# Kernel optimization log

Hardware: AMD Instinct MI355X
Metric: run time of the kernel (lower is better)

Reference implementation:

```python
import jax, jax.numpy as jnp
import numpy as np

N = 50000      # nodes
E = 800000     # edges (avg degree 16)
D = 64         # input/hidden dim
OUT = 1        # output head dim
ATT_SLOPE = 0.2   # PyG GATConv leaky_relu slope for attention logits
ACT_SLOPE = 0.01  # nn.LeakyReLU default slope


def _gat_layer(x, src, dst, W, a_src, a_dst, b, n):
    """PyG GATConv, heads=1, concat=True, with self-loops already in src/dst."""
    h = x @ W.T                                   # [n, D]
    logit = jax.nn.leaky_relu(h[src] @ a_src + h[dst] @ a_dst, ATT_SLOPE)  # [e]
    m = jax.ops.segment_max(logit, dst, num_segments=n)                    # per-dst max
    e = jnp.exp(logit - m[dst])
    denom = jax.ops.segment_sum(e, dst, num_segments=n)
    coef = e / denom[dst]                         # softmax over incoming edges
    out = jax.ops.segment_sum(coef[:, None] * h[src], dst, num_segments=n)
    return out + b


def setup_inputs() -> dict:
    key = jax.random.key(0)
    ks = jax.random.split(key, 16)
    s = 1.0 / np.sqrt(D)
    inp = {"x": jax.random.normal(ks[0], (N, D), dtype=jnp.float32)}
    for i in range(3):
        inp[f"W{i}"] = jax.random.normal(ks[1 + 4 * i], (D, D), dtype=jnp.float32) * s
        inp[f"a_src{i}"] = jax.random.normal(ks[2 + 4 * i], (D,), dtype=jnp.float32) * s
        inp[f"a_dst{i}"] = jax.random.normal(ks[3 + 4 * i], (D,), dtype=jnp.float32) * s
        inp[f"b{i}"] = jnp.zeros((D,), dtype=jnp.float32)
    inp["Wout"] = jax.random.normal(ks[13], (OUT, D), dtype=jnp.float32) * s
    inp["bout"] = jnp.zeros((OUT,), dtype=jnp.float32)
    inp["edge_index"] = jax.random.randint(ks[14], (2, E), 0, N, dtype=jnp.int64)
    return inp


def reference(x, W0, a_src0, a_dst0, b0, W1, a_src1, a_dst1, b1,
              W2, a_src2, a_dst2, b2, Wout, bout, edge_index):
    n = x.shape[0]
    loops = jnp.arange(n, dtype=edge_index.dtype)
    src = jnp.concatenate([edge_index[0], loops])  # GATConv add_self_loops=True
    dst = jnp.concatenate([edge_index[1], loops])
    act = lambda v: jax.nn.leaky_relu(v, ACT_SLOPE)
    h = act(_gat_layer(x, src, dst, W0, a_src0, a_dst0, b0, n))
    h = act(_gat_layer(h, src, dst, W1, a_src1, a_dst1, b1, n))
    h = act(_gat_layer(h, src, dst, W2, a_src2, a_dst2, b2, n))
    return h @ Wout.T + bout                       # [n, OUT]
```

## Files before the change

### kernel.cpp

```cpp
#include <hip/hip_runtime.h>
#include <hip/hip_fp16.h>

#define DD 64
#define ATT_SLOPE 0.2f
#define ACT_SLOPE 0.01f
#define GNPB 32
#define RCAP 64
#define PA_CHUNK 2048
#define BSH 8
#define BNODES 256
#define BCAP 5888

template <bool IN_HALF>
__device__ __forceinline__ void gemm_body(
        const void* __restrict__ in_, const float* __restrict__ W,
        const float* __restrict__ a_src, const float* __restrict__ a_dst,
        __half* __restrict__ h, float* __restrict__ as_out,
        float* __restrict__ ad_out, int n_nodes, int base, float* xin) {
    int t = threadIdx.x;
    int lane = t & 63;
    int w = t >> 6;
    if (IN_HALF) {
        const uint2* src = (const uint2*)in_;
        float4* xin4 = (float4*)xin;
        int lim = n_nodes * (DD / 4);
        #pragma unroll
        for (int i = 0; i < 2; ++i) {
            int idx = i * 256 + t;
            int gi = base * (DD / 4) + idx;
            uint2 v = {0, 0};
            if (gi < lim) v = src[gi];
            float2 f0 = __half22float2(*(const __half2*)&v.x);
            float2 f1 = __half22float2(*(const __half2*)&v.y);
            xin4[idx] = make_float4(f0.x, f0.y, f1.x, f1.y);
        }
    } else {
        float4* xin4 = (float4*)xin;
        const float4* src4 = (const float4*)in_;
        int lim = n_nodes * (DD / 4);
        #pragma unroll
        for (int i = 0; i < (GNPB * DD / 4) / 256; ++i) {
            int idx = i * 256 + t;
            int gi = base * (DD / 4) + idx;
            xin4[idx] = (gi < lim) ? src4[gi]
                                   : make_float4(0.f, 0.f, 0.f, 0.f);
        }
    }
    __syncthreads();

    int n0 = base + w * 8;
    if (n0 >= n_nodes) return;

    float asl = a_src[lane], adl = a_dst[lane];
    const float* wrow = W + (size_t)lane * 64;
    int rmax = n_nodes - n0; if (rmax > 8) rmax = 8;

    if (rmax == 8) {
        float a[8] = {0.f, 0.f, 0.f, 0.f, 0.f, 0.f, 0.f, 0.f};
        #pragma unroll
        for (int kq = 0; kq < 16; ++kq) {
            float4 wv = *(const float4*)(wrow + kq * 4);
            #pragma unroll
            for (int r = 0; r < 8; ++r) {
                float4 xv = *(const float4*)&xin[(w * 8 + r) * DD + kq * 4];
                a[r] = fmaf(xv.x, wv.x, a[r]); a[r] = fmaf(xv.y, wv.y, a[r]);
                a[r] = fmaf(xv.z, wv.z, a[r]); a[r] = fmaf(xv.w, wv.w, a[r]);
            }
        }
        #pragma unroll
        for (int r = 0; r < 8; ++r)
            h[(size_t)(n0 + r) * 64 + lane] = __float2half(a[r]);
        float s[16];
        #pragma unroll
        for (int r = 0; r < 8; ++r) { s[2 * r] = a[r] * asl; s[2 * r + 1] = a[r] * adl; }
        #pragma unroll
        for (int m = 32; m >= 1; m >>= 1) {
            #pragma unroll
            for (int i = 0; i < 16; ++i) s[i] += __shfl_xor(s[i], m, 64);
        }
        if (lane == 0) {
            #pragma unroll
            for (int r = 0; r < 8; ++r) {
                as_out[n0 + r] = s[2 * r];
                ad_out[n0 + r] = s[2 * r + 1];
            }
        }
    } else {
        for (int r = 0; r < rmax; ++r) {
            int node = n0 + r;
            float acc = 0.f;
            #pragma unroll
            for (int kq = 0; kq < 16; ++kq) {
                float4 wv = *(const float4*)(wrow + kq * 4);
                float4 xv = *(const float4*)&xin[(w * 8 + r) * DD + kq * 4];
                acc = fmaf(xv.x, wv.x, acc); acc = fmaf(xv.y, wv.y, acc);
                acc = fmaf(xv.z, wv.z, acc); acc = fmaf(xv.w, wv.w, acc);
            }
            h[(size_t)node * 64 + lane] = __float2half(acc);
            float s1 = acc * asl, s2 = acc * adl;
            #pragma unroll
            for (int m = 32; m >= 1; m >>= 1) {
                s1 += __shfl_xor(s1, m, 64);
                s2 += __shfl_xor(s2, m, 64);
            }
            if (lane == 0) { as_out[node] = s1; ad_out[node] = s2; }
        }
    }
}

__global__ __launch_bounds__(256) void gemm0_binA_kernel(
        const float* __restrict__ x, const float* __restrict__ W,
        const float* __restrict__ a_src, const float* __restrict__ a_dst,
        __half* __restrict__ h, float* __restrict__ as_out,
        float* __restrict__ ad_out, int n_nodes,
        const int* __restrict__ ei, int E,
        int* __restrict__ bcur, unsigned int* __restrict__ bucket_buf,
        int bin_blocks) {
    __shared__ float xin[GNPB * DD];
    int* hist  = (int*)xin;
    int* gbase = hist + 256;
    int bid = blockIdx.x;
    if (bid >= bin_blocks) {
        gemm_body<false>(x, W, a_src, a_dst, h, as_out, ad_out, n_nodes,
                         (bid - bin_blocks) * GNPB, xin);
        return;
    }
    int t = threadIdx.x;
    int base_e = bid * PA_CHUNK;
    int ET = E + n_nodes;
    hist[t] = 0;
    __syncthreads();

    unsigned int ent[8];
    short eb[8];
    short ep[8];
    #pragma unroll
    for (int j = 0; j < 8; ++j) {
        int e = base_e + j * 256 + t;
        eb[j] = -1;
        if (e >= ET) continue;
        int s, d;
        if (e < E) { s = ei[e]; d = ei[E + e]; }
        else       { s = e - E; d = s; }
        int b = d >> BSH;
        ent[j] = (unsigned int)s | ((unsigned int)(d & (BNODES - 1)) << 16);
        eb[j] = (short)b;
        ep[j] = (short)atomicAdd(&hist[b], 1);
    }
    __syncthreads();
    {
        int c = hist[t];
        gbase[t] = (c > 0) ? atomicAdd(&bcur[t], c) : 0;
    }
    __syncthreads();
    #pragma unroll
    for (int j = 0; j < 8; ++j) {
        if (eb[j] < 0) continue;
        int pos = gbase[eb[j]] + ep[j];
        if (pos < BCAP) bucket_buf[(size_t)eb[j] * BCAP + pos] = ent[j];
    }
}

__global__ __launch_bounds__(256) void binB_kernel(
        const unsigned int* __restrict__ bucket_buf, const int* __restrict__ bcur,
        int* __restrict__ counts, unsigned short* __restrict__ col_src,
        int n_nodes) {
    __shared__ int cur[BNODES];
    int b = blockIdx.x, t = threadIdx.x;
    if (t < BNODES) cur[t] = 0;
    __syncthreads();
    int cnt = bcur[b]; if (cnt > BCAP) cnt = BCAP;
    const unsigned int* buf = bucket_buf + (size_t)b * BCAP;
    for (int i = t; i < cnt; i += 256) {
        unsigned int en = buf[i];
        int s = en & 0xFFFF;
        int dl = en >> 16;
        int pos = atomicAdd(&cur[dl], 1);
        if (pos < RCAP)
            col_src[(((b << BSH) + dl) << 6) + pos] = (unsigned short)s;
    }
    __syncthreads();
    int n0 = b << BSH;
    if (t < BNODES) {
        int d = n0 + t;
        if (d < n_nodes) counts[d] = cur[t];
    }
}

__global__ __launch_bounds__(256) void gemm_alpha_kernel(
        const __half* __restrict__ in, const float* __restrict__ W,
        const float* __restrict__ a_src, const float* __restrict__ a_dst,
        __half* __restrict__ h, float* __restrict__ as_out,
        float* __restrict__ ad_out, int n_nodes) {
    __shared__ float xin[GNPB * DD];
    gemm_body<true>(in, W, a_src, a_dst, h, as_out, ad_out, n_nodes,
                    blockIdx.x * GNPB, xin);
}

template <bool FUSE_HEAD>
__global__ __launch_bounds__(256) void aggregate_kernel(
        const int* __restrict__ counts, const unsigned short* __restrict__ col_src,
        const __half* __restrict__ h, const float* __restrict__ as_arr,
        const float* __restrict__ ad_arr, const float* __restrict__ b,
        __half* __restrict__ out16, float* __restrict__ head_out,
        const float* __restrict__ Wout, const float* __restrict__ bout,
        int n_nodes) {
    int t = threadIdx.x;
    int w = t >> 6, lane = t & 63;
    int node = blockIdx.x * 4 + w;
    if (node >= n_nodes) return;
    int g = lane >> 3, u = lane & 7;

    int beg = node << 6;
    int cnt = __builtin_amdgcn_readfirstlane(counts[node]);
    if (cnt > RCAP) cnt = RCAP;
    int end = beg + cnt;
    float adn = ad_arr[node];

    float acc[8] = {0.f, 0.f, 0.f, 0.f, 0.f, 0.f, 0.f, 0.f};
    float lsum = 0.f;
    int e = beg + g;

    uint4 rA = {0, 0, 0, 0}, rB = {0, 0, 0, 0};
    float aA = 0.f, aB = 0.f;
    if (e < end) {
        int s = col_src[e];
        aA = as_arr[s];
        rA = *(const uint4*)(h + (size_t)s * 64 + u * 8);
    }
    if (e + 8 < end) {
        int s = col_src[e + 8];
        aB = as_arr[s];
        rB = *(const uint4*)(h + (size_t)s * 64 + u * 8);
    }
    while (e < end) {
        int e2 = e + 16;
        uint4 rC = {0, 0, 0, 0}; float aC = 0.f;
        if (e2 < end) {
            int s = col_src[e2];
            aC = as_arr[s];
            rC = *(const uint4*)(h + (size_t)s * 64 + u * 8);
        }
        float lg = aA + adn;
        lg = (lg >= 0.f) ? lg : ATT_SLOPE * lg;
        float p = __expf(lg);
        lsum += p;
        float2 f0 = __half22float2(*(const __half2*)&rA.x);
        float2 f1 = __half22float2(*(const __half2*)&rA.y);
        float2 f2 = __half22float2(*(const __half2*)&rA.z);
        float2 f3 = __half22float2(*(const __half2*)&rA.w);
        acc[0] = fmaf(p, f0.x, acc[0]); acc[1] = fmaf(p, f0.y, acc[1]);
        acc[2] = fmaf(p, f1.x, acc[2]); acc[3] = fmaf(p, f1.y, acc[3]);
        acc[4] = fmaf(p, f2.x, acc[4]); acc[5] = fmaf(p, f2.y, acc[5]);
        acc[6] = fmaf(p, f3.x, acc[6]); acc[7] = fmaf(p, f3.y, acc[7]);
        rA = rB; aA = aB;
        rB = rC; aB = aC;
        e += 8;
    }
    #pragma unroll
    for (int m = 8; m <= 32; m <<= 1) {
        #pragma unroll
        for (int i = 0; i < 8; ++i) acc[i] += __shfl_xor(acc[i], m, 64);
        lsum += __shfl_xor(lsum, m, 64);
    }
    float inv = 1.f / lsum;
    const float4 b0 = *(const float4*)(b + u * 8);
    const float4 b1 = *(const float4*)(b + u * 8 + 4);
    float o[8];
    o[0] = acc[0] * inv + b0.x; o[1] = acc[1] * inv + b0.y;
    o[2] = acc[2] * inv + b0.z; o[3] = acc[3] * inv + b0.w;
    o[4] = acc[4] * inv + b1.x; o[5] = acc[5] * inv + b1.y;
    o[6] = acc[6] * inv + b1.z; o[7] = acc[7] * inv + b1.w;
    #pragma unroll
    for (int i = 0; i < 8; ++i) o[i] = (o[i] >= 0.f) ? o[i] : ACT_SLOPE * o[i];

    if (FUSE_HEAD) {
        const float4 w0 = *(const float4*)(Wout + u * 8);
        const float4 w1 = *(const float4*)(Wout + u * 8 + 4);
        float pd = o[0] * w0.x + o[1] * w0.y + o[2] * w0.z + o[3] * w0.w
                 + o[4] * w1.x + o[5] * w1.y + o[6] * w1.z + o[7] * w1.w;
        #pragma unroll
        for (int m = 1; m <= 4; m <<= 1) pd += __shfl_xor(pd, m, 64);
        if (lane == 0) head_out[node] = pd + bout[0];
    } else if (g == 0) {
        __half2 p0 = __floats2half2_rn(o[0], o[1]);
        __half2 p1 = __floats2half2_rn(o[2], o[3]);
        __half2 p2 = __floats2half2_rn(o[4], o[5]);
        __half2 p3 = __floats2half2_rn(o[6], o[7]);
        uint4 pv;
        pv.x = *(unsigned int*)&p0; pv.y = *(unsigned int*)&p1;
        pv.z = *(unsigned int*)&p2; pv.w = *(unsigned int*)&p3;
        *(uint4*)(out16 + ((size_t)node << 6) + u * 8) = pv;
    }
}


extern "C" void kernel_launch(void* const* d_in, const int* in_sizes, int n_in,
                              void* d_out, int out_size, void* d_ws, size_t ws_size,
                              hipStream_t stream) {
    const float* x     = (const float*)d_in[0];
    const float* W[3]  = {(const float*)d_in[1], (const float*)d_in[5], (const float*)d_in[9]};
    const float* as[3] = {(const float*)d_in[2], (const float*)d_in[6], (const float*)d_in[10]};
    const float* ad[3] = {(const float*)d_in[3], (const float*)d_in[7], (const float*)d_in[11]};
    const float* bv[3] = {(const float*)d_in[4], (const float*)d_in[8], (const float*)d_in[12]};
    const float* Wout  = (const float*)d_in[13];
    const float* bout  = (const float*)d_in[14];
    const int*   ei    = (const int*)d_in[15];

    const int N  = in_sizes[0] / DD;
    const int E  = in_sizes[15] / 2;
    const int ET = E + N;
    const int NBUCK = (N + BNODES - 1) >> BSH;

    char* ws = (char*)d_ws;
    size_t off = 0;
    auto alloc = [&](size_t bytes) {
        void* p = ws + off;
        off = (off + bytes + 255) & ~(size_t)255;
        return p;
    };
    unsigned short* col_src = (unsigned short*)alloc((size_t)N * RCAP * 2);
    int*    counts  = (int*)alloc((size_t)N * 4);
    int*    bcur    = (int*)alloc(256 * 4);
    float*  asA     = (float*)alloc((size_t)N * 4);
    float*  adA     = (float*)alloc((size_t)N * 4);
    float*  asB     = (float*)alloc((size_t)N * 4);
    float*  adB     = (float*)alloc((size_t)N * 4);
    __half* hA      = (__half*)alloc((size_t)N * DD * 2);
    __half* hB      = (__half*)alloc((size_t)N * DD * 2);
    __half* obuf16  = (__half*)alloc((size_t)N * DD * 2);
    unsigned int* bucket_buf = (unsigned int*)alloc((size_t)NBUCK * BCAP * 4);
    (void)ws_size;

    int gridG = (N + GNPB - 1) / GNPB;
    int nA    = (ET + PA_CHUNK - 1) / PA_CHUNK;
    int grid4 = (N + 3) / 4;

    hipMemsetAsync(bcur, 0, 256 * 4, stream);
    gemm0_binA_kernel<<<gridG + nA, 256, 0, stream>>>(
        x, W[0], as[0], ad[0], hA, asA, adA, N,
        ei, E, bcur, bucket_buf, nA);
    binB_kernel<<<NBUCK, 256, 0, stream>>>(bucket_buf, bcur, counts, col_src, N);

    aggregate_kernel<false><<<grid4, 256, 0, stream>>>(
        counts, col_src, hA, asA, adA, bv[0], obuf16,
        nullptr, nullptr, nullptr, N);
    gemm_alpha_kernel<<<gridG, 256, 0, stream>>>(obuf16, W[1], as[1], ad[1],
                                                 hB, asB, adB, N);
    aggregate_kernel<false><<<grid4, 256, 0, stream>>>(
        counts, col_src, hB, asB, adB, bv[1], obuf16,
        nullptr, nullptr, nullptr, N);
    gemm_alpha_kernel<<<gridG, 256, 0, stream>>>(obuf16, W[2], as[2], ad[2],
                                                 hA, asA, adA, N);
    aggregate_kernel<true><<<grid4, 256, 0, stream>>>(
        counts, col_src, hA, asA, adA, bv[2], nullptr,
        (float*)d_out, Wout, bout, N);
}
```

Baseline: 251.6 us.

## Fuse layer aggregation with next layer's linear transform and attention projections

Merges the aggregate kernel and the following GEMM/alpha kernel into one kernel. Each wavefront aggregates 8 nodes in sequence, places the activated fp32 results in shared memory, then applies the next layer's W and the attention vectors directly. This drops the fp16 intermediate buffer round trip and two kernel launches. The cost is that each block now handles 32 nodes with a serial per-node loop, which lowers per-node parallelism during the gather and may hurt latency hiding.

```diff
diff --git a/kernel.cpp b/kernel.cpp
--- a/kernel.cpp
+++ b/kernel.cpp
@@ -11,40 +11,23 @@
 #define BNODES 256
 #define BCAP 5888
 
-template <bool IN_HALF>
 __device__ __forceinline__ void gemm_body(
-        const void* __restrict__ in_, const float* __restrict__ W,
+        const float* __restrict__ in, const float* __restrict__ W,
         const float* __restrict__ a_src, const float* __restrict__ a_dst,
         __half* __restrict__ h, float* __restrict__ as_out,
         float* __restrict__ ad_out, int n_nodes, int base, float* xin) {
     int t = threadIdx.x;
     int lane = t & 63;
     int w = t >> 6;
-    if (IN_HALF) {
-        const uint2* src = (const uint2*)in_;
-        float4* xin4 = (float4*)xin;
-        int lim = n_nodes * (DD / 4);
-        #pragma unroll
-        for (int i = 0; i < 2; ++i) {
-            int idx = i * 256 + t;
-            int gi = base * (DD / 4) + idx;
-            uint2 v = {0, 0};
-            if (gi < lim) v = src[gi];
-            float2 f0 = __half22float2(*(const __half2*)&v.x);
-            float2 f1 = __half22float2(*(const __half2*)&v.y);
-            xin4[idx] = make_float4(f0.x, f0.y, f1.x, f1.y);
-        }
-    } else {
-        float4* xin4 = (float4*)xin;
-        const float4* src4 = (const float4*)in_;
-        int lim = n_nodes * (DD / 4);
-        #pragma unroll
-        for (int i = 0; i < (GNPB * DD / 4) / 256; ++i) {
-            int idx = i * 256 + t;
-            int gi = base * (DD / 4) + idx;
-            xin4[idx] = (gi < lim) ? src4[gi]
-                                   : make_float4(0.f, 0.f, 0.f, 0.f);
-        }
+    float4* xin4 = (float4*)xin;
+    const float4* src4 = (const float4*)in;
+    int lim = n_nodes * (DD / 4);
+    #pragma unroll
+    for (int i = 0; i < (GNPB * DD / 4) / 256; ++i) {
+        int idx = i * 256 + t;
+        int gi = base * (DD / 4) + idx;
+        xin4[idx] = (gi < lim) ? src4[gi]
+                               : make_float4(0.f, 0.f, 0.f, 0.f);
     }
     __syncthreads();
 
@@ -121,8 +104,8 @@
     int* gbase = hist + 256;
     int bid = blockIdx.x;
     if (bid >= bin_blocks) {
-        gemm_body<false>(x, W, a_src, a_dst, h, as_out, ad_out, n_nodes,
-                         (bid - bin_blocks) * GNPB, xin);
+        gemm_body(x, W, a_src, a_dst, h, as_out, ad_out, n_nodes,
+                  (bid - bin_blocks) * GNPB, xin);
         return;
     }
     int t = threadIdx.x;
@@ -187,22 +170,163 @@
     }
 }
 
-__global__ __launch_bounds__(256) void gemm_alpha_kernel(
-        const __half* __restrict__ in, const float* __restrict__ W,
-        const float* __restrict__ a_src, const float* __restrict__ a_dst,
-        __half* __restrict__ h, float* __restrict__ as_out,
-        float* __restrict__ ad_out, int n_nodes) {
-    __shared__ float xin[GNPB * DD];
-    gemm_body<true>(in, W, a_src, a_dst, h, as_out, ad_out, n_nodes,
-                    blockIdx.x * GNPB, xin);
-}
-
-template <bool FUSE_HEAD>
-__global__ __launch_bounds__(256) void aggregate_kernel(
+__global__ __launch_bounds__(256) void fused_agg_gemm_kernel(
         const int* __restrict__ counts, const unsigned short* __restrict__ col_src,
         const __half* __restrict__ h, const float* __restrict__ as_arr,
         const float* __restrict__ ad_arr, const float* __restrict__ b,
-        __half* __restrict__ out16, float* __restrict__ head_out,
+        const float* __restrict__ Wn, const float* __restrict__ an_src,
+        const float* __restrict__ an_dst, __half* __restrict__ h_next,
+        float* __restrict__ as_next, float* __restrict__ ad_next,
+        int n_nodes) {
+    __shared__ float xin[GNPB * DD];
+    int t = threadIdx.x;
+    int w = t >> 6, lane = t & 63;
+    int g = lane >> 3, u = lane & 7;
+    int n0 = blockIdx.x * GNPB + w * 8;
+    int nloc = n_nodes - n0;
+    if (nloc > 8) nloc = 8;
+    if (nloc < 0) nloc = 0;
+
+    int cn = 0; float adp = 0.f;
+    {
+        int idx = n0 + (lane & 7);
+        if (idx < n_nodes) { cn = counts[idx]; adp = ad_arr[idx]; }
+    }
+    const float4 b0 = *(const float4*)(b + u * 8);
+    const float4 b1 = *(const float4*)(b + u * 8 + 4);
+
+    for (int r = 0; r < nloc; ++r) {
+        int node = n0 + r;
+        int cnt = __shfl(cn, r, 64);
+        if (cnt > RCAP) cnt = RCAP;
+        float adn = __shfl(adp, r, 64);
+        int beg = node << 6;
+        int end = beg + cnt;
+
+        float acc[8] = {0.f, 0.f, 0.f, 0.f, 0.f, 0.f, 0.f, 0.f};
+        float lsum = 0.f;
+        int e = beg + g;
+
+        uint4 rA = {0, 0, 0, 0}, rB = {0, 0, 0, 0};
+        float aA = 0.f, aB = 0.f;
+        if (e < end) {
+            int s = col_src[e];
+            aA = as_arr[s];
+            rA = *(const uint4*)(h + (size_t)s * 64 + u * 8);
+        }
+        if (e + 8 < end) {
+            int s = col_src[e + 8];
+            aB = as_arr[s];
+            rB = *(const uint4*)(h + (size_t)s * 64 + u * 8);
+        }
+        while (e < end) {
+            int e2 = e + 16;
+            uint4 rC = {0, 0, 0, 0}; float aC = 0.f;
+            if (e2 < end) {
+                int s = col_src[e2];
+                aC = as_arr[s];
+                rC = *(const uint4*)(h + (size_t)s * 64 + u * 8);
+            }
+            float lg = aA + adn;
+            lg = (lg >= 0.f) ? lg : ATT_SLOPE * lg;
+            float p = __expf(lg);
+            lsum += p;
+            float2 f0 = __half22float2(*(const __half2*)&rA.x);
+            float2 f1 = __half22float2(*(const __half2*)&rA.y);
+            float2 f2 = __half22float2(*(const __half2*)&rA.z);
+            float2 f3 = __half22float2(*(const __half2*)&rA.w);
+            acc[0] = fmaf(p, f0.x, acc[0]); acc[1] = fmaf(p, f0.y, acc[1]);
+            acc[2] = fmaf(p, f1.x, acc[2]); acc[3] = fmaf(p, f1.y, acc[3]);
+            acc[4] = fmaf(p, f2.x, acc[4]); acc[5] = fmaf(p, f2.y, acc[5]);
+            acc[6] = fmaf(p, f3.x, acc[6]); acc[7] = fmaf(p, f3.y, acc[7]);
+            rA = rB; aA = aB;
+            rB = rC; aB = aC;
+            e += 8;
+        }
+        #pragma unroll
+        for (int m = 8; m <= 32; m <<= 1) {
+            #pragma unroll
+            for (int i = 0; i < 8; ++i) acc[i] += __shfl_xor(acc[i], m, 64);
+            lsum += __shfl_xor(lsum, m, 64);
+        }
+        float inv = 1.f / lsum;
+        float o[8];
+        o[0] = acc[0] * inv + b0.x; o[1] = acc[1] * inv + b0.y;
+        o[2] = acc[2] * inv + b0.z; o[3] = acc[3] * inv + b0.w;
+        o[4] = acc[4] * inv + b1.x; o[5] = acc[5] * inv + b1.y;
+        o[6] = acc[6] * inv + b1.z; o[7] = acc[7] * inv + b1.w;
+        #pragma unroll
+        for (int i = 0; i < 8; ++i) o[i] = (o[i] >= 0.f) ? o[i] : ACT_SLOPE * o[i];
+        if (g == 0) {
+            float4* row = (float4*)&xin[(w * 8 + r) * DD + u * 8];
+            row[0] = make_float4(o[0], o[1], o[2], o[3]);
+            row[1] = make_float4(o[4], o[5], o[6], o[7]);
+        }
+    }
+    __syncthreads();
+
+    if (nloc == 0) return;
+    float asl = an_src[lane], adl = an_dst[lane];
+    const float* wrow = Wn + (size_t)lane * 64;
+
+    if (nloc == 8) {
+        float a[8] = {0.f, 0.f, 0.f, 0.f, 0.f, 0.f, 0.f, 0.f};
+        #pragma unroll
+        for (int kq = 0; kq < 16; ++kq) {
+            float4 wv = *(const float4*)(wrow + kq * 4);
+            #pragma unroll
+            for (int r = 0; r < 8; ++r) {
+                float4 xv = *(const float4*)&xin[(w * 8 + r) * DD + kq * 4];
+                a[r] = fmaf(xv.x, wv.x, a[r]); a[r] = fmaf(xv.y, wv.y, a[r]);
+                a[r] = fmaf(xv.z, wv.z, a[r]); a[r] = fmaf(xv.w, wv.w, a[r]);
+            }
+        }
+        #pragma unroll
+        for (int r = 0; r < 8; ++r)
+            h_next[(size_t)(n0 + r) * 64 + lane] = __float2half(a[r]);
+        float s[16];
+        #pragma unroll
+        for (int r = 0; r < 8; ++r) { s[2 * r] = a[r] * asl; s[2 * r + 1] = a[r] * adl; }
+        #pragma unroll
+        for (int m = 32; m >= 1; m >>= 1) {
+            #pragma unroll
+            for (int i = 0; i < 16; ++i) s[i] += __shfl_xor(s[i], m, 64);
+        }
+        if (lane == 0) {
+            #pragma unroll
+            for (int r = 0; r < 8; ++r) {
+                as_next[n0 + r] = s[2 * r];
+                ad_next[n0 + r] = s[2 * r + 1];
+            }
+        }
+    } else {
+        for (int r = 0; r < nloc; ++r) {
+            int node = n0 + r;
+            float acc = 0.f;
+            #pragma unroll
+            for (int kq = 0; kq < 16; ++kq) {
+                float4 wv = *(const float4*)(wrow + kq * 4);
+                float4 xv = *(const float4*)&xin[(w * 8 + r) * DD + kq * 4];
+                acc = fmaf(xv.x, wv.x, acc); acc = fmaf(xv.y, wv.y, acc);
+                acc = fmaf(xv.z, wv.z, acc); acc = fmaf(xv.w, wv.w, acc);
+            }
+            h_next[(size_t)node * 64 + lane] = __float2half(acc);
+            float s1 = acc * asl, s2 = acc * adl;
+            #pragma unroll
+            for (int m = 32; m >= 1; m >>= 1) {
+                s1 += __shfl_xor(s1, m, 64);
+                s2 += __shfl_xor(s2, m, 64);
+            }
+            if (lane == 0) { as_next[node] = s1; ad_next[node] = s2; }
+        }
+    }
+}
+
+__global__ __launch_bounds__(256) void aggregate_head_kernel(
+        const int* __restrict__ counts, const unsigned short* __restrict__ col_src,
+        const __half* __restrict__ h, const float* __restrict__ as_arr,
+        const float* __restrict__ ad_arr, const float* __restrict__ b,
+        float* __restrict__ head_out,
         const float* __restrict__ Wout, const float* __restrict__ bout,
         int n_nodes) {
     int t = threadIdx.x;
@@ -274,24 +398,13 @@
     #pragma unroll
     for (int i = 0; i < 8; ++i) o[i] = (o[i] >= 0.f) ? o[i] : ACT_SLOPE * o[i];
 
-    if (FUSE_HEAD) {
-        const float4 w0 = *(const float4*)(Wout + u * 8);
-        const float4 w1 = *(const float4*)(Wout + u * 8 + 4);
-        float pd = o[0] * w0.x + o[1] * w0.y + o[2] * w0.z + o[3] * w0.w
-                 + o[4] * w1.x + o[5] * w1.y + o[6] * w1.z + o[7] * w1.w;
-        #pragma unroll
-        for (int m = 1; m <= 4; m <<= 1) pd += __shfl_xor(pd, m, 64);
-        if (lane == 0) head_out[node] = pd + bout[0];
-    } else if (g == 0) {
-        __half2 p0 = __floats2half2_rn(o[0], o[1]);
-        __half2 p1 = __floats2half2_rn(o[2], o[3]);
-        __half2 p2 = __floats2half2_rn(o[4], o[5]);
-        __half2 p3 = __floats2half2_rn(o[6], o[7]);
-        uint4 pv;
-        pv.x = *(unsigned int*)&p0; pv.y = *(unsigned int*)&p1;
-        pv.z = *(unsigned int*)&p2; pv.w = *(unsigned int*)&p3;
-        *(uint4*)(out16 + ((size_t)node << 6) + u * 8) = pv;
-    }
+    const float4 w0 = *(const float4*)(Wout + u * 8);
+    const float4 w1 = *(const float4*)(Wout + u * 8 + 4);
+    float pd = o[0] * w0.x + o[1] * w0.y + o[2] * w0.z + o[3] * w0.w
+             + o[4] * w1.x + o[5] * w1.y + o[6] * w1.z + o[7] * w1.w;
+    #pragma unroll
+    for (int m = 1; m <= 4; m <<= 1) pd += __shfl_xor(pd, m, 64);
+    if (lane == 0) head_out[node] = pd + bout[0];
 }
 
 
@@ -328,7 +441,6 @@
     float*  adB     = (float*)alloc((size_t)N * 4);
     __half* hA      = (__half*)alloc((size_t)N * DD * 2);
     __half* hB      = (__half*)alloc((size_t)N * DD * 2);
-    __half* obuf16  = (__half*)alloc((size_t)N * DD * 2);
     unsigned int* bucket_buf = (unsigned int*)alloc((size_t)NBUCK * BCAP * 4);
     (void)ws_size;
 
@@ -342,17 +454,13 @@
         ei, E, bcur, bucket_buf, nA);
     binB_kernel<<<NBUCK, 256, 0, stream>>>(bucket_buf, bcur, counts, col_src, N);
 
-    aggregate_kernel<false><<<grid4, 256, 0, stream>>>(
-        counts, col_src, hA, asA, adA, bv[0], obuf16,
-        nullptr, nullptr, nullptr, N);
-    gemm_alpha_kernel<<<gridG, 256, 0, stream>>>(obuf16, W[1], as[1], ad[1],
-                                                 hB, asB, adB, N);
-    aggregate_kernel<false><<<grid4, 256, 0, stream>>>(
-        counts, col_src, hB, asB, adB, bv[1], obuf16,
-        nullptr, nullptr, nullptr, N);
-    gemm_alpha_kernel<<<gridG, 256, 0, stream>>>(obuf16, W[2], as[2], ad[2],
-                                                 hA, asA, adA, N);
-    aggregate_kernel<true><<<grid4, 256, 0, stream>>>(
-        counts, col_src, hA, asA, adA, bv[2], nullptr,
+    fused_agg_gemm_kernel<<<gridG, 256, 0, stream>>>(
+        counts, col_src, hA, asA, adA, bv[0],
+        W[1], as[1], ad[1], hB, asB, adB, N);
+    fused_agg_gemm_kernel<<<gridG, 256, 0, stream>>>(
+        counts, col_src, hB, asB, adB, bv[1],
+        W[2], as[2], ad[2], hA, asA, adA, N);
+    aggregate_head_kernel<<<grid4, 256, 0, stream>>>(
+        counts, col_src, hA, asA, adA, bv[2],
         (float*)d_out, Wout, bout, N);
 }
```

New measurement: 262.1 us. 4.2% more time.

## Map one node per 8-lane group in aggregation instead of one per wavefront

Applied to the files above, without the earlier changes.

The aggregation kernel now gives each 8-lane group its own destination node, so a wavefront handles 8 nodes and a block handles 32. Each group walks its node's edges serially with a three-deep prefetch. This removes the cross-group shuffle reduction and the idle lanes in wavefronts whose nodes have few edges. In exchange, loop trip counts diverge across the groups in a wavefront, since nodes differ in degree. Each group also processes edges one at a time, which lengthens the serial dependency chain per node.

```diff
diff --git a/kernel.cpp b/kernel.cpp
--- a/kernel.cpp
+++ b/kernel.cpp
@@ -207,39 +207,43 @@
         int n_nodes) {
     int t = threadIdx.x;
     int w = t >> 6, lane = t & 63;
-    int node = blockIdx.x * 4 + w;
-    if (node >= n_nodes) return;
     int g = lane >> 3, u = lane & 7;
-
-    int beg = node << 6;
-    int cnt = __builtin_amdgcn_readfirstlane(counts[node]);
+    int node = blockIdx.x * GNPB + w * 8 + g;
+    bool valid = node < n_nodes;
+
+    int cnt = 0; float adn = 0.f;
+    if (valid) { cnt = counts[node]; adn = ad_arr[node]; }
     if (cnt > RCAP) cnt = RCAP;
-    int end = beg + cnt;
-    float adn = ad_arr[node];
+    int e   = node << 6;
+    int end = e + cnt;
 
     float acc[8] = {0.f, 0.f, 0.f, 0.f, 0.f, 0.f, 0.f, 0.f};
     float lsum = 0.f;
-    int e = beg + g;
-
-    uint4 rA = {0, 0, 0, 0}, rB = {0, 0, 0, 0};
-    float aA = 0.f, aB = 0.f;
+
+    uint4 rA = {0,0,0,0}, rB = {0,0,0,0}, rC = {0,0,0,0};
+    float aA = 0.f, aB = 0.f, aC = 0.f;
     if (e < end) {
         int s = col_src[e];
         aA = as_arr[s];
         rA = *(const uint4*)(h + (size_t)s * 64 + u * 8);
     }
-    if (e + 8 < end) {
-        int s = col_src[e + 8];
+    if (e + 1 < end) {
+        int s = col_src[e + 1];
         aB = as_arr[s];
         rB = *(const uint4*)(h + (size_t)s * 64 + u * 8);
     }
+    if (e + 2 < end) {
+        int s = col_src[e + 2];
+        aC = as_arr[s];
+        rC = *(const uint4*)(h + (size_t)s * 64 + u * 8);
+    }
     while (e < end) {
-        int e2 = e + 16;
-        uint4 rC = {0, 0, 0, 0}; float aC = 0.f;
-        if (e2 < end) {
-            int s = col_src[e2];
-            aC = as_arr[s];
-            rC = *(const uint4*)(h + (size_t)s * 64 + u * 8);
+        int e3 = e + 3;
+        uint4 rD = {0,0,0,0}; float aD = 0.f;
+        if (e3 < end) {
+            int s = col_src[e3];
+            aD = as_arr[s];
+            rD = *(const uint4*)(h + (size_t)s * 64 + u * 8);
         }
         float lg = aA + adn;
         lg = (lg >= 0.f) ? lg : ATT_SLOPE * lg;
@@ -255,13 +259,8 @@
         acc[6] = fmaf(p, f3.x, acc[6]); acc[7] = fmaf(p, f3.y, acc[7]);
         rA = rB; aA = aB;
         rB = rC; aB = aC;
-        e += 8;
-    }
-    #pragma unroll
-    for (int m = 8; m <= 32; m <<= 1) {
-        #pragma unroll
-        for (int i = 0; i < 8; ++i) acc[i] += __shfl_xor(acc[i], m, 64);
-        lsum += __shfl_xor(lsum, m, 64);
+        rC = rD; aC = aD;
+        ++e;
     }
     float inv = 1.f / lsum;
     const float4 b0 = *(const float4*)(b + u * 8);
@@ -279,10 +278,11 @@
         const float4 w1 = *(const float4*)(Wout + u * 8 + 4);
         float pd = o[0] * w0.x + o[1] * w0.y + o[2] * w0.z + o[3] * w0.w
                  + o[4] * w1.x + o[5] * w1.y + o[6] * w1.z + o[7] * w1.w;
-        #pragma unroll
-        for (int m = 1; m <= 4; m <<= 1) pd += __shfl_xor(pd, m, 64);
-        if (lane == 0) head_out[node] = pd + bout[0];
-    } else if (g == 0) {
+        pd += __shfl_xor(pd, 1, 64);
+        pd += __shfl_xor(pd, 2, 64);
+        pd += __shfl_xor(pd, 4, 64);
+        if (valid && u == 0) head_out[node] = pd + bout[0];
+    } else if (valid) {
         __half2 p0 = __floats2half2_rn(o[0], o[1]);
         __half2 p1 = __floats2half2_rn(o[2], o[3]);
         __half2 p2 = __floats2half2_rn(o[4], o[5]);
@@ -334,7 +334,6 @@
 
     int gridG = (N + GNPB - 1) / GNPB;
     int nA    = (ET + PA_CHUNK - 1) / PA_CHUNK;
-    int grid4 = (N + 3) / 4;
 
     hipMemsetAsync(bcur, 0, 256 * 4, stream);
     gemm0_binA_kernel<<<gridG + nA, 256, 0, stream>>>(
@@ -342,17 +341,17 @@
         ei, E, bcur, bucket_buf, nA);
     binB_kernel<<<NBUCK, 256, 0, stream>>>(bucket_buf, bcur, counts, col_src, N);
 
-    aggregate_kernel<false><<<grid4, 256, 0, stream>>>(
+    aggregate_kernel<false><<<gridG, 256, 0, stream>>>(
         counts, col_src, hA, asA, adA, bv[0], obuf16,
         nullptr, nullptr, nullptr, N);
     gemm_alpha_kernel<<<gridG, 256, 0, stream>>>(obuf16, W[1], as[1], ad[1],
                                                  hB, asB, adB, N);
-    aggregate_kernel<false><<<grid4, 256, 0, stream>>>(
+    aggregate_kernel<false><<<gridG, 256, 0, stream>>>(
         counts, col_src, hB, asB, adB, bv[1], obuf16,
         nullptr, nullptr, nullptr, N);
     gemm_alpha_kernel<<<gridG, 256, 0, stream>>>(obuf16, W[2], as[2], ad[2],
                                                  hA, asA, adA, N);
-    aggregate_kernel<true><<<grid4, 256, 0, stream>>>(
+    aggregate_kernel<true><<<gridG, 256, 0, stream>>>(
         counts, col_src, hA, asA, adA, bv[2], nullptr,
         (float*)d_out, Wout, bout, N);
 }
```

New measurement: 252.4 us. About the same (+0.3%).
